# Optimization experiments

Measured on AMD Instinct MI355X. Metric: run time of the kernel, lower is better.

## Reference

```python
import jax, jax.numpy as jnp
import numpy as np

T_LEN, BATCH = 256, 256
HID, OUT = 1024, 768


def setup_inputs() -> dict:
    key = jax.random.key(0)
    ks = jax.random.split(key, 8)
    s = 0.02
    return {
        "src": jax.random.normal(ks[0], (2, BATCH, OUT), jnp.float32),
        "tgt": jax.random.randint(ks[1], (T_LEN, BATCH), 0, 30000, jnp.int64),
        "hidden": jax.random.normal(ks[2], (1, BATCH, HID), jnp.float32),
        "W_ih": jax.random.normal(ks[3], (3 * HID, OUT), jnp.float32) * s,
        "W_hh": jax.random.normal(ks[4], (3 * HID, HID), jnp.float32) * s,
        "b_ih": jnp.zeros((3 * HID,), jnp.float32),
        "b_hh": jnp.zeros((3 * HID,), jnp.float32),
        "W_fc": jax.random.normal(ks[5], (OUT, HID), jnp.float32) * s,
        "b_fc": jnp.zeros((OUT,), jnp.float32),
    }


def reference(src, tgt, hidden, W_ih, W_hh, b_ih, b_hh, W_fc, b_fc):
    tgt_len = tgt.shape[0]
    x0 = src[0]          # [B, OUT] first decoder input
    h0 = hidden[0]       # [B, HID] single-layer GRU state

    def step(carry, _):
        x, h = carry
        gi = x @ W_ih.T + b_ih          # [B, 3H]
        gh = h @ W_hh.T + b_hh          # [B, 3H]
        i_r, i_z, i_n = jnp.split(gi, 3, axis=-1)
        h_r, h_z, h_n = jnp.split(gh, 3, axis=-1)
        r = jax.nn.sigmoid(i_r + h_r)
        z = jax.nn.sigmoid(i_z + h_z)
        n = jnp.tanh(i_n + r * h_n)
        h_new = (1.0 - z) * n + z * h
        y = h_new @ W_fc.T + b_fc       # [B, OUT], fed back next step
        return (y, h_new), y

    _, outputs = jax.lax.scan(step, (x0, h0), None, length=tgt_len)
    return outputs  # [tgt_len, B, OUT]
```

## Files before the change

kernel.cpp:

```cpp
#include <hip/hip_runtime.h>

typedef _Float16 f16;
typedef __attribute__((ext_vector_type(8))) _Float16 f16x8;
typedef __attribute__((ext_vector_type(16))) float f32x16;

#define MFMA32 __builtin_amdgcn_mfma_f32_32x32x16_f16

#define TLEN 256
#define BATCH 256
#define HIDN 1024
#define OUTD 768

static constexpr int SMEM_BYTES = (8*4352 + 64*68) * 4;

__device__ __forceinline__ f16x8 ldf(const f16* p){
  return *reinterpret_cast<const f16x8*>(p);
}
__device__ __forceinline__ float sigm(float x){ return 1.0f/(1.0f + __expf(-x)); }
__device__ __forceinline__ float tanh_(float x){ return 1.0f - 2.0f/(1.0f + __expf(2.0f*x)); }

__device__ __forceinline__ void reduce_to_F(float* red, float* F,
    const f32x16 (&acc)[2][2], int w, int lo, int hi, int tid)
{
  #pragma unroll
  for (int mt = 0; mt < 2; ++mt){
    #pragma unroll
    for (int nt = 0; nt < 2; ++nt){
      int n = nt*32 + lo;
      #pragma unroll
      for (int q = 0; q < 4; ++q){
        int slot = mt*8 + 2*q + hi;
        float4 v = make_float4(acc[mt][nt][4*q+0], acc[mt][nt][4*q+1],
                               acc[mt][nt][4*q+2], acc[mt][nt][4*q+3]);
        *reinterpret_cast<float4*>(red + w*4352 + n*68 + slot*4) = v;
      }
    }
  }
  __syncthreads();
  int n = tid >> 3, mqb = tid & 7;
  #pragma unroll
  for (int hh = 0; hh < 2; ++hh){
    int mq = mqb + hh*8;
    float4 s = make_float4(0.f, 0.f, 0.f, 0.f);
    #pragma unroll
    for (int w2 = 0; w2 < 8; ++w2){
      float4 v = *reinterpret_cast<const float4*>(red + w2*4352 + n*68 + mq*4);
      s.x += v.x; s.y += v.y; s.z += v.z; s.w += v.w;
    }
    int m0 = mq*4;
    F[(m0+0)*68 + n] = s.x;
    F[(m0+1)*68 + n] = s.y;
    F[(m0+2)*68 + n] = s.z;
    F[(m0+3)*68 + n] = s.w;
  }
  __syncthreads();
}

__device__ __forceinline__ void gates_epilogue(const float* F, const float* bias,
    float* h32, f16* hOut, int bb, int cc, int tid)
{
  int b = tid >> 3, hu2 = (tid & 7)*2;
  #pragma unroll
  for (int u = 0; u < 2; ++u){
    int hu_l = hu2 + u;
    float4 g4 = *reinterpret_cast<const float4*>(F + b*68 + hu_l*4);
    float4 bi = *reinterpret_cast<const float4*>(bias + cc*64 + hu_l*4);
    float r  = sigm(g4.x + bi.x);
    float z  = sigm(g4.y + bi.y);
    float nn = tanh_(g4.z + bi.z + r*(g4.w + bi.w));
    size_t idx = (size_t)(bb*64 + b)*HIDN + (size_t)cc*16 + hu_l;
    float hold = h32[idx];
    float hn = (1.0f - z)*nn + z*hold;
    h32[idx] = hn;
    hOut[idx] = (f16)hn;
  }
}

__global__ __launch_bounds__(512, 2) void step_kernel(
    const f16* __restrict__ A, const f16* __restrict__ W,
    const float* __restrict__ bias, float* __restrict__ h32,
    f16* __restrict__ hOut)
{
  extern __shared__ float smem[];
  float* red = smem;
  float* F = smem + 8*4352;
  int tid = threadIdx.x;
  int w = tid >> 6, l = tid & 63, lo = l & 31, hi = l >> 5;
  int bb = blockIdx.x >> 6, cc = blockIdx.x & 63;
  int k0 = w*128 + hi*8;

  f16x8 bf[8][2];
  #pragma unroll
  for (int ks = 0; ks < 8; ++ks){
    #pragma unroll
    for (int nt = 0; nt < 2; ++nt)
      bf[ks][nt] = ldf(W + (size_t)(cc*64 + nt*32 + lo)*HIDN + k0 + ks*16);
  }
  f32x16 zero = {0,0,0,0,0,0,0,0,0,0,0,0,0,0,0,0};
  f32x16 acc[2][2];
  acc[0][0]=zero; acc[0][1]=zero; acc[1][0]=zero; acc[1][1]=zero;

  const f16* Ab = A + (size_t)(bb*64 + lo)*HIDN + k0;
  #pragma unroll
  for (int ks = 0; ks < 8; ++ks){
    f16x8 a0 = ldf(Ab + ks*16);
    f16x8 a1 = ldf(Ab + (size_t)32*HIDN + ks*16);
    acc[0][0] = MFMA32(a0, bf[ks][0], acc[0][0], 0, 0, 0);
    acc[0][1] = MFMA32(a0, bf[ks][1], acc[0][1], 0, 0, 0);
    acc[1][0] = MFMA32(a1, bf[ks][0], acc[1][0], 0, 0, 0);
    acc[1][1] = MFMA32(a1, bf[ks][1], acc[1][1], 0, 0, 0);
  }
  reduce_to_F(red, F, acc, w, lo, hi, tid);
  gates_epilogue(F, bias, h32, hOut, bb, cc, tid);
}

__global__ __launch_bounds__(512, 2) void step0_kernel(
    const f16* __restrict__ X0, const f16* __restrict__ H0,
    const f16* __restrict__ Wih, const f16* __restrict__ Whh,
    const float* __restrict__ bias0, float* __restrict__ h32,
    f16* __restrict__ hOut)
{
  extern __shared__ float smem[];
  float* red = smem;
  float* F = smem + 8*4352;
  int tid = threadIdx.x;
  int w = tid >> 6, l = tid & 63, lo = l & 31, hi = l >> 5;
  int bb = blockIdx.x >> 6, cc = blockIdx.x & 63;
  int k0w = w*224;

  f16x8 bf[14][2];
  #pragma unroll
  for (int ks = 0; ks < 14; ++ks){
    #pragma unroll
    for (int nt = 0; nt < 2; ++nt){
      int jl = nt*32 + lo;
      int g = jl & 3, hu = cc*16 + (jl >> 2);
      int kb = k0w + ks*16;
      int kk = kb + hi*8;
      f16x8 v = {0,0,0,0,0,0,0,0};
      if (kb < 768){
        if (g < 3) v = ldf(Wih + (size_t)(g*1024 + hu)*768 + kk);
      } else {
        if (g != 2) v = ldf(Whh + (size_t)(((g==3)?2:g)*1024 + hu)*1024 + (kk - 768));
      }
      bf[ks][nt] = v;
    }
  }
  f32x16 zero = {0,0,0,0,0,0,0,0,0,0,0,0,0,0,0,0};
  f32x16 acc[2][2];
  acc[0][0]=zero; acc[0][1]=zero; acc[1][0]=zero; acc[1][1]=zero;

  #pragma unroll
  for (int ks = 0; ks < 14; ++ks){
    int kb = k0w + ks*16;
    f16x8 a0, a1;
    if (kb < 768){
      int kk = kb + hi*8;
      a0 = ldf(X0 + (size_t)(bb*64 + lo)*768 + kk);
      a1 = ldf(X0 + (size_t)(bb*64 + 32 + lo)*768 + kk);
    } else {
      int kk = kb - 768 + hi*8;
      a0 = ldf(H0 + (size_t)(bb*64 + lo)*HIDN + kk);
      a1 = ldf(H0 + (size_t)(bb*64 + 32 + lo)*HIDN + kk);
    }
    acc[0][0] = MFMA32(a0, bf[ks][0], acc[0][0], 0, 0, 0);
    acc[0][1] = MFMA32(a0, bf[ks][1], acc[0][1], 0, 0, 0);
    acc[1][0] = MFMA32(a1, bf[ks][0], acc[1][0], 0, 0, 0);
    acc[1][1] = MFMA32(a1, bf[ks][1], acc[1][1], 0, 0, 0);
  }
  reduce_to_F(red, F, acc, w, lo, hi, tid);
  gates_epilogue(F, bias0, h32, hOut, bb, cc, tid);
}

__global__ __launch_bounds__(512, 2) void wc_gemm(
    const f16* __restrict__ Aih, const f16* __restrict__ BfcT,
    const float* __restrict__ Whh, f16* __restrict__ Wstep)
{
  extern __shared__ float smem[];
  float* red = smem;
  float* F = smem + 8*4352;
  int tid = threadIdx.x;
  int w = tid >> 6, l = tid & 63, lo = l & 31, hi = l >> 5;
  int mb = blockIdx.x >> 4, nb = blockIdx.x & 15;
  int k0 = w*96 + hi*8;

  f16x8 bf[6][2];
  #pragma unroll
  for (int ks = 0; ks < 6; ++ks){
    #pragma unroll
    for (int nt = 0; nt < 2; ++nt)
      bf[ks][nt] = ldf(BfcT + (size_t)(nb*64 + nt*32 + lo)*768 + k0 + ks*16);
  }
  f32x16 zero = {0,0,0,0,0,0,0,0,0,0,0,0,0,0,0,0};
  f32x16 acc[2][2];
  acc[0][0]=zero; acc[0][1]=zero; acc[1][0]=zero; acc[1][1]=zero;

  const f16* Ab = Aih + (size_t)(mb*64 + lo)*768 + k0;
  #pragma unroll
  for (int ks = 0; ks < 6; ++ks){
    f16x8 a0 = ldf(Ab + ks*16);
    f16x8 a1 = ldf(Ab + (size_t)32*768 + ks*16);
    acc[0][0] = MFMA32(a0, bf[ks][0], acc[0][0], 0, 0, 0);
    acc[0][1] = MFMA32(a0, bf[ks][1], acc[0][1], 0, 0, 0);
    acc[1][0] = MFMA32(a1, bf[ks][0], acc[1][0], 0, 0, 0);
    acc[1][1] = MFMA32(a1, bf[ks][1], acc[1][1], 0, 0, 0);
  }
  reduce_to_F(red, F, acc, w, lo, hi, tid);

  int m_l = tid >> 3, n0 = (tid & 7)*8;
  int m = mb*64 + m_l;
  int g = m >> 10, hu = m & 1023;
  int row = (hu >> 4)*64 + ((hu & 15) << 2) + g;
  f16x8 ov;
  #pragma unroll
  for (int i = 0; i < 8; ++i){
    float v = F[m_l*68 + n0 + i];
    if (g < 2) v += Whh[(size_t)m*1024 + nb*64 + n0 + i];
    ov[i] = (f16)v;
  }
  *reinterpret_cast<f16x8*>(Wstep + (size_t)row*HIDN + nb*64 + n0) = ov;
}

__global__ __launch_bounds__(512, 2) void y_gemm(
    const f16* __restrict__ H, const f16* __restrict__ Wfc,
    const float* __restrict__ bfc, float* __restrict__ out)
{
  extern __shared__ float smem[];
  float* red = smem;
  float* F = smem + 8*4352;
  int tid = threadIdx.x;
  int w = tid >> 6, l = tid & 63, lo = l & 31, hi = l >> 5;
  int mb = blockIdx.x / 12, ob = blockIdx.x % 12;
  int k0 = w*128 + hi*8;

  f16x8 bf[8][2];
  #pragma unroll
  for (int ks = 0; ks < 8; ++ks){
    #pragma unroll
    for (int nt = 0; nt < 2; ++nt)
      bf[ks][nt] = ldf(Wfc + (size_t)(ob*64 + nt*32 + lo)*HIDN + k0 + ks*16);
  }
  f32x16 zero = {0,0,0,0,0,0,0,0,0,0,0,0,0,0,0,0};
  f32x16 acc[2][2];
  acc[0][0]=zero; acc[0][1]=zero; acc[1][0]=zero; acc[1][1]=zero;

  const f16* Ab = H + (size_t)(mb*64 + lo)*HIDN + k0;
  #pragma unroll
  for (int ks = 0; ks < 8; ++ks){
    f16x8 a0 = ldf(Ab + ks*16);
    f16x8 a1 = ldf(Ab + (size_t)32*HIDN + ks*16);
    acc[0][0] = MFMA32(a0, bf[ks][0], acc[0][0], 0, 0, 0);
    acc[0][1] = MFMA32(a0, bf[ks][1], acc[0][1], 0, 0, 0);
    acc[1][0] = MFMA32(a1, bf[ks][0], acc[1][0], 0, 0, 0);
    acc[1][1] = MFMA32(a1, bf[ks][1], acc[1][1], 0, 0, 0);
  }
  reduce_to_F(red, F, acc, w, lo, hi, tid);

  int m_l = tid >> 3, n0 = (tid & 7)*8;
  float* po = out + (size_t)(mb*64 + m_l)*OUTD + ob*64 + n0;
  float4 v0 = make_float4(F[m_l*68+n0+0] + bfc[ob*64+n0+0],
                          F[m_l*68+n0+1] + bfc[ob*64+n0+1],
                          F[m_l*68+n0+2] + bfc[ob*64+n0+2],
                          F[m_l*68+n0+3] + bfc[ob*64+n0+3]);
  float4 v1 = make_float4(F[m_l*68+n0+4] + bfc[ob*64+n0+4],
                          F[m_l*68+n0+5] + bfc[ob*64+n0+5],
                          F[m_l*68+n0+6] + bfc[ob*64+n0+6],
                          F[m_l*68+n0+7] + bfc[ob*64+n0+7]);
  *reinterpret_cast<float4*>(po) = v0;
  *reinterpret_cast<float4*>(po + 4) = v1;
}

__global__ void cast_all(const float* __restrict__ Wih, const float* __restrict__ Wfc,
    const float* __restrict__ Whh, const float* __restrict__ src,
    const float* __restrict__ hidden,
    f16* __restrict__ Wih16, f16* __restrict__ Wfc16, f16* __restrict__ WfcT16,
    f16* __restrict__ Whh16, f16* __restrict__ X016, f16* __restrict__ H016,
    float* __restrict__ h32)
{
  const int S0 = 3072*768, S1 = 768*1024, S2 = 3072*1024, S3 = 256*768, S4 = 256*1024;
  const int total = S0 + S1 + S2 + S3 + S4;
  for (int i = blockIdx.x*blockDim.x + threadIdx.x; i < total; i += gridDim.x*blockDim.x){
    int j = i;
    if (j < S0){ Wih16[j] = (f16)Wih[j]; continue; }
    j -= S0;
    if (j < S1){
      float v = Wfc[j];
      Wfc16[j] = (f16)v;
      int o = j >> 10, k = j & 1023;
      WfcT16[(size_t)k*768 + o] = (f16)v;
      continue;
    }
    j -= S1;
    if (j < S2){ Whh16[j] = (f16)Whh[j]; continue; }
    j -= S2;
    if (j < S3){ X016[j] = (f16)src[j]; continue; }
    j -= S3;
    float v = hidden[j];
    h32[j] = v;
    H016[j] = (f16)v;
  }
}

__global__ void pack_hn(const float* __restrict__ Whh, f16* __restrict__ Wstep){
  int i = blockIdx.x*blockDim.x + threadIdx.x;
  int hu = i >> 7, kq = (i & 127) << 3;
  const float* p = Whh + (size_t)(2048 + hu)*1024 + kq;
  f16x8 ov;
  #pragma unroll
  for (int j = 0; j < 8; ++j) ov[j] = (f16)p[j];
  int row = (hu >> 4)*64 + ((hu & 15) << 2) + 3;
  *reinterpret_cast<f16x8*>(Wstep + (size_t)row*HIDN + kq) = ov;
}

__global__ void bias_kernel(const float* __restrict__ Wih, const float* __restrict__ bih,
    const float* __restrict__ bhh, const float* __restrict__ bfc,
    float* __restrict__ bias, float* __restrict__ bias0)
{
  int r = blockIdx.x*4 + (threadIdx.x >> 6);
  int l = threadIdx.x & 63;
  int j = r & 63, cc = r >> 6;
  int g = j & 3, hu = cc*16 + (j >> 2);
  float dot = 0.f;
  if (g < 3){
    int m = g*1024 + hu;
    for (int i = l; i < 768; i += 64) dot += Wih[(size_t)m*768 + i] * bfc[i];
    #pragma unroll
    for (int off = 32; off > 0; off >>= 1) dot += __shfl_down(dot, off);
  }
  if (l == 0){
    float bv, b0v;
    if (g < 2){ int m = g*1024 + hu; bv = bih[m] + dot + bhh[m]; b0v = bih[m] + bhh[m]; }
    else if (g == 2){ int m = 2048 + hu; bv = bih[m] + dot; b0v = bih[m]; }
    else { bv = bhh[2048 + hu]; b0v = bv; }
    bias[r] = bv;
    bias0[r] = b0v;
  }
}

extern "C" void kernel_launch(void* const* d_in, const int* in_sizes, int n_in,
                              void* d_out, int out_size, void* d_ws, size_t ws_size,
                              hipStream_t stream)
{
  const float* src    = (const float*)d_in[0];
  const float* hidden = (const float*)d_in[2];
  const float* W_ih   = (const float*)d_in[3];
  const float* W_hh   = (const float*)d_in[4];
  const float* b_ih   = (const float*)d_in[5];
  const float* b_hh   = (const float*)d_in[6];
  const float* W_fc   = (const float*)d_in[7];
  const float* b_fc   = (const float*)d_in[8];
  float* out = (float*)d_out;
  char* ws = (char*)d_ws;

  size_t o = 0;
  f16* Wstep  = (f16*)(ws + o); o += (size_t)4096*1024*2;
  f16* Wih16  = (f16*)(ws + o); o += (size_t)3072*768*2;
  f16* Wfc16  = (f16*)(ws + o); o += (size_t)768*1024*2;
  f16* WfcT16 = (f16*)(ws + o); o += (size_t)1024*768*2;
  f16* Whh16  = (f16*)(ws + o); o += (size_t)3072*1024*2;
  f16* X016   = (f16*)(ws + o); o += (size_t)256*768*2;
  f16* H016   = (f16*)(ws + o); o += (size_t)256*1024*2;
  float* h32  = (float*)(ws + o); o += (size_t)256*1024*4;
  float* bias = (float*)(ws + o); o += (size_t)4096*4;
  float* bias0= (float*)(ws + o); o += (size_t)4096*4;
  f16* hist   = (f16*)(ws + o); o += (size_t)TLEN*BATCH*HIDN*2;

  (void)hipFuncSetAttribute(reinterpret_cast<const void*>(step_kernel),
      hipFuncAttributeMaxDynamicSharedMemorySize, SMEM_BYTES);
  (void)hipFuncSetAttribute(reinterpret_cast<const void*>(step0_kernel),
      hipFuncAttributeMaxDynamicSharedMemorySize, SMEM_BYTES);
  (void)hipFuncSetAttribute(reinterpret_cast<const void*>(wc_gemm),
      hipFuncAttributeMaxDynamicSharedMemorySize, SMEM_BYTES);
  (void)hipFuncSetAttribute(reinterpret_cast<const void*>(y_gemm),
      hipFuncAttributeMaxDynamicSharedMemorySize, SMEM_BYTES);

  cast_all<<<4096, 256, 0, stream>>>(W_ih, W_fc, W_hh, src, hidden,
      Wih16, Wfc16, WfcT16, Whh16, X016, H016, h32);
  bias_kernel<<<1024, 256, 0, stream>>>(W_ih, b_ih, b_hh, b_fc, bias, bias0);
  wc_gemm<<<768, 512, SMEM_BYTES, stream>>>(Wih16, WfcT16, W_hh, Wstep);
  pack_hn<<<512, 256, 0, stream>>>(W_hh, Wstep);

  step0_kernel<<<256, 512, SMEM_BYTES, stream>>>(X016, H016, Wih16, Whh16, bias0, h32, hist);
  for (int t = 1; t < TLEN; ++t){
    step_kernel<<<256, 512, SMEM_BYTES, stream>>>(
        hist + (size_t)(t-1)*BATCH*HIDN, Wstep, bias, h32,
        hist + (size_t)t*BATCH*HIDN);
  }
  y_gemm<<<12288, 512, SMEM_BYTES, stream>>>(hist, Wfc16, b_fc, out);
}
```

Measured before the change: 3.683 ms.

## Replace per-step kernel launches with persistent cooperative kernel and batch-group flags

The 255 separate step launches become one cooperative persistent kernel. Each block keeps its slice of the step weights in registers across all timesteps and waits on a per-batch-group atomic counter, so only the 64 blocks sharing a batch slice synchronize with each other. The GRU hidden state is carried in registers rather than reloaded from global memory. This removes launch overhead and repeated weight loads, but relies on all 256 blocks being co-resident and on spin-wait flags with acquire/release fences for correctness.

```diff
diff --git a/kernel.cpp b/kernel.cpp
--- a/kernel.cpp
+++ b/kernel.cpp
@@ -12,6 +12,7 @@
 #define OUTD 768
 
 static constexpr int SMEM_BYTES = (8*4352 + 64*68) * 4;
+static constexpr int PSMEM_BYTES = 98304;
 
 __device__ __forceinline__ f16x8 ldf(const f16* p){
   return *reinterpret_cast<const f16x8*>(p);
@@ -76,43 +77,100 @@
   }
 }
 
-__global__ __launch_bounds__(512, 2) void step_kernel(
-    const f16* __restrict__ A, const f16* __restrict__ W,
-    const float* __restrict__ bias, float* __restrict__ h32,
-    f16* __restrict__ hOut)
-{
-  extern __shared__ float smem[];
-  float* red = smem;
-  float* F = smem + 8*4352;
+__global__ __launch_bounds__(512, 2) void gru_persistent(
+    f16* __restrict__ hist, const f16* __restrict__ Wstep,
+    const float* __restrict__ bias, const float* __restrict__ h32init,
+    unsigned int* __restrict__ ctr)
+{
+  extern __shared__ float part[];
   int tid = threadIdx.x;
   int w = tid >> 6, l = tid & 63, lo = l & 31, hi = l >> 5;
-  int bb = blockIdx.x >> 6, cc = blockIdx.x & 63;
-  int k0 = w*128 + hi*8;
-
-  f16x8 bf[8][2];
-  #pragma unroll
-  for (int ks = 0; ks < 8; ++ks){
-    #pragma unroll
-    for (int nt = 0; nt < 2; ++nt)
-      bf[ks][nt] = ldf(W + (size_t)(cc*64 + nt*32 + lo)*HIDN + k0 + ks*16);
-  }
-  f32x16 zero = {0,0,0,0,0,0,0,0,0,0,0,0,0,0,0,0};
-  f32x16 acc[2][2];
-  acc[0][0]=zero; acc[0][1]=zero; acc[1][0]=zero; acc[1][1]=zero;
-
-  const f16* Ab = A + (size_t)(bb*64 + lo)*HIDN + k0;
-  #pragma unroll
-  for (int ks = 0; ks < 8; ++ks){
-    f16x8 a0 = ldf(Ab + ks*16);
-    f16x8 a1 = ldf(Ab + (size_t)32*HIDN + ks*16);
-    acc[0][0] = MFMA32(a0, bf[ks][0], acc[0][0], 0, 0, 0);
-    acc[0][1] = MFMA32(a0, bf[ks][1], acc[0][1], 0, 0, 0);
-    acc[1][0] = MFMA32(a1, bf[ks][0], acc[1][0], 0, 0, 0);
-    acc[1][1] = MFMA32(a1, bf[ks][1], acc[1][1], 0, 0, 0);
-  }
-  reduce_to_F(red, F, acc, w, lo, hi, tid);
-  gates_epilogue(F, bias, h32, hOut, bb, cc, tid);
-}
+  int wk = w & 3, wm = w >> 2;
+  int bb = blockIdx.x & 3, cc = blockIdx.x >> 2;
+  unsigned int* ctrb = ctr + bb*64;
+
+  const f16* Wb = Wstep + (size_t)(cc*64 + lo)*HIDN + wk*256 + hi*8;
+  f16x8 bw0[16], bw1[16];
+  #pragma unroll
+  for (int kc = 0; kc < 16; ++kc){
+    bw0[kc] = ldf(Wb + kc*16);
+    bw1[kc] = ldf(Wb + (size_t)32*HIDN + kc*16);
+  }
+
+  int em = tid >> 3, e = tid & 7;
+  int wmg = em >> 5, ml = em & 31;
+  float4 bi0 = *reinterpret_cast<const float4*>(bias + cc*64 + e*8);
+  float4 bi1 = *reinterpret_cast<const float4*>(bias + cc*64 + e*8 + 4);
+  size_t hrow = (size_t)(bb*64 + em)*HIDN + (size_t)cc*16 + 2*e;
+  float hold0 = h32init[hrow];
+  float hold1 = h32init[hrow + 1];
+
+  const f32x16 Z = {0,0,0,0,0,0,0,0,0,0,0,0,0,0,0,0};
+
+  for (int t = 1; t < TLEN; ++t){
+    if (t > 1){
+      if (tid == 0){
+        unsigned target = 64u * (unsigned)(t - 1);
+        while (__hip_atomic_load(ctrb, __ATOMIC_RELAXED, __HIP_MEMORY_SCOPE_AGENT) < target)
+          __builtin_amdgcn_s_sleep(2);
+        __builtin_amdgcn_fence(__ATOMIC_ACQUIRE, "agent");
+      }
+      __syncthreads();
+    }
+
+    const f16* Ab = hist + (size_t)(t-1)*BATCH*HIDN
+                  + (size_t)(bb*64 + wm*32 + lo)*HIDN + wk*256 + hi*8;
+    f32x16 acc0 = Z, acc1 = Z;
+    #pragma unroll
+    for (int kc = 0; kc < 16; ++kc){
+      f16x8 a = ldf(Ab + kc*16);
+      acc0 = MFMA32(a, bw0[kc], acc0, 0, 0, 0);
+      acc1 = MFMA32(a, bw1[kc], acc1, 0, 0, 0);
+    }
+
+    float* pw = part + w*2176;
+    #pragma unroll
+    for (int r = 0; r < 16; ++r){
+      int m_l = (r & 3) + 8*(r >> 2) + 4*hi;
+      pw[m_l*68 + lo]      = acc0[r];
+      pw[m_l*68 + 32 + lo] = acc1[r];
+    }
+    __syncthreads();
+
+    const float* pb = part + (size_t)wmg*4*2176 + ml*68 + e*8;
+    float4 g0 = make_float4(0.f,0.f,0.f,0.f), g1 = make_float4(0.f,0.f,0.f,0.f);
+    #pragma unroll
+    for (int j = 0; j < 4; ++j){
+      const float* q = pb + j*2176;
+      float4 a = *reinterpret_cast<const float4*>(q);
+      float4 b = *reinterpret_cast<const float4*>(q + 4);
+      g0.x += a.x; g0.y += a.y; g0.z += a.z; g0.w += a.w;
+      g1.x += b.x; g1.y += b.y; g1.z += b.z; g1.w += b.w;
+    }
+    float r0 = sigm(g0.x + bi0.x), z0 = sigm(g0.y + bi0.y);
+    float n0 = tanh_(g0.z + bi0.z + r0*(g0.w + bi0.w));
+    float hn0 = (1.f - z0)*n0 + z0*hold0; hold0 = hn0;
+    float r1 = sigm(g1.x + bi1.x), z1 = sigm(g1.y + bi1.y);
+    float n1 = tanh_(g1.z + bi1.z + r1*(g1.w + bi1.w));
+    float hn1 = (1.f - z1)*n1 + z1*hold1; hold1 = hn1;
+
+    unsigned short u0 = __builtin_bit_cast(unsigned short, (f16)hn0);
+    unsigned short u1 = __builtin_bit_cast(unsigned short, (f16)hn1);
+    unsigned pk = (unsigned)u0 | ((unsigned)u1 << 16);
+    __hip_atomic_store(
+        reinterpret_cast<unsigned*>(hist + (size_t)t*BATCH*HIDN + hrow),
+        pk, __ATOMIC_RELAXED, __HIP_MEMORY_SCOPE_AGENT);
+
+    __syncthreads();
+
+    if (t < TLEN-1 && tid == 0){
+      __builtin_amdgcn_fence(__ATOMIC_RELEASE, "agent");
+      __hip_atomic_fetch_add(ctrb, 1u, __ATOMIC_RELAXED, __HIP_MEMORY_SCOPE_AGENT);
+    }
+  }
+}
+
+__global__ void init_ctr(unsigned int* c){ c[threadIdx.x] = 0u; }
 
 __global__ __launch_bounds__(512, 2) void step0_kernel(
     const f16* __restrict__ X0, const f16* __restrict__ H0,
@@ -364,27 +422,29 @@
   float* bias = (float*)(ws + o); o += (size_t)4096*4;
   float* bias0= (float*)(ws + o); o += (size_t)4096*4;
   f16* hist   = (f16*)(ws + o); o += (size_t)TLEN*BATCH*HIDN*2;
-
-  (void)hipFuncSetAttribute(reinterpret_cast<const void*>(step_kernel),
-      hipFuncAttributeMaxDynamicSharedMemorySize, SMEM_BYTES);
+  unsigned int* ctr = (unsigned int*)(ws + o); o += 256*4;
+
   (void)hipFuncSetAttribute(reinterpret_cast<const void*>(step0_kernel),
       hipFuncAttributeMaxDynamicSharedMemorySize, SMEM_BYTES);
   (void)hipFuncSetAttribute(reinterpret_cast<const void*>(wc_gemm),
       hipFuncAttributeMaxDynamicSharedMemorySize, SMEM_BYTES);
   (void)hipFuncSetAttribute(reinterpret_cast<const void*>(y_gemm),
       hipFuncAttributeMaxDynamicSharedMemorySize, SMEM_BYTES);
+  (void)hipFuncSetAttribute(reinterpret_cast<const void*>(gru_persistent),
+      hipFuncAttributeMaxDynamicSharedMemorySize, PSMEM_BYTES);
 
   cast_all<<<4096, 256, 0, stream>>>(W_ih, W_fc, W_hh, src, hidden,
       Wih16, Wfc16, WfcT16, Whh16, X016, H016, h32);
   bias_kernel<<<1024, 256, 0, stream>>>(W_ih, b_ih, b_hh, b_fc, bias, bias0);
   wc_gemm<<<768, 512, SMEM_BYTES, stream>>>(Wih16, WfcT16, W_hh, Wstep);
   pack_hn<<<512, 256, 0, stream>>>(W_hh, Wstep);
+  init_ctr<<<1, 256, 0, stream>>>(ctr);
 
   step0_kernel<<<256, 512, SMEM_BYTES, stream>>>(X016, H016, Wih16, Whh16, bias0, h32, hist);
-  for (int t = 1; t < TLEN; ++t){
-    step_kernel<<<256, 512, SMEM_BYTES, stream>>>(
-        hist + (size_t)(t-1)*BATCH*HIDN, Wstep, bias, h32,
-        hist + (size_t)t*BATCH*HIDN);
-  }
+
+  void* pargs[] = { (void*)&hist, (void*)&Wstep, (void*)&bias, (void*)&h32, (void*)&ctr };
+  (void)hipLaunchCooperativeKernel(reinterpret_cast<void*>(gru_persistent),
+      dim3(256), dim3(512), pargs, PSMEM_BYTES, stream);
+
   y_gemm<<<12288, 512, SMEM_BYTES, stream>>>(hist, Wfc16, b_fc, out);
 }
```

Result: faster. 3.256 ms (-11.6%).
